# Optimization experiments

Hardware: AMD Instinct MI355X
Metric: run time of the kernel (lower is better)

The kernel has to match this reference:

```python
import jax, jax.numpy as jnp
import numpy as np

B, T, S, D, H, DK, DV = 4, 2048, 2048, 1024, 16, 64, 64


def setup_inputs() -> dict:
    key = jax.random.key(0)
    ks = jax.random.split(key, 12)
    sq = 1.0 / np.sqrt(D)
    return {
        "query": jax.random.normal(ks[0], (B, T, D), jnp.float32),
        "value": jax.random.normal(ks[1], (B, S, D), jnp.float32),
        "mask": jnp.ones((B, T, S), dtype=bool),
        "Wq": jax.random.normal(ks[2], (D, H, DK), jnp.float32) * sq,
        "bq": jnp.zeros((H, DK), jnp.float32),
        "Wk": jax.random.normal(ks[3], (D, H, DK), jnp.float32) * sq,
        "bk": jnp.zeros((H, DK), jnp.float32),
        "Wv": jax.random.normal(ks[4], (D, H, DV), jnp.float32) * sq,
        "bv": jnp.zeros((H, DV), jnp.float32),
        "Wo": jax.random.normal(ks[5], (H, DV, D), jnp.float32) * (1.0 / np.sqrt(H * DV)),
        "bo": jnp.zeros((D,), jnp.float32),
    }


def reference(query, value, mask, Wq, bq, Wk, bk, Wv, bv, Wo, bo):
    # key input defaults to value when only [query, value] is given
    q = jnp.einsum("btd,dhk->bthk", query, Wq) + bq  # [B,T,H,DK]
    k = jnp.einsum("bsd,dhk->bshk", value, Wk) + bk  # [B,S,H,DK]
    v = jnp.einsum("bsd,dhv->bshv", value, Wv) + bv  # [B,S,H,DV]
    # dot_product_equation 'aecd,abcd->acbe': scores[b,h,t,s]
    scores = jnp.einsum("bshk,bthk->bhts", k, q) * (1.0 / np.sqrt(DK))
    # MaskedSoftmax: mask [B,T,S] expanded at axis 1 -> [B,1,T,S]
    adder = (1.0 - mask[:, None, :, :].astype(scores.dtype)) * -10000.0
    probs = jax.nn.softmax(scores + adder, axis=-1)
    # combine_equation 'acbe,aecd->abcd'
    attn = jnp.einsum("bhts,bshv->bthv", probs, v)  # [B,T,H,DV]
    out = jnp.einsum("bthv,hvd->btd", attn, Wo) + bo  # [B,T,D]
    return out
```

## Files before the change

kernel.cpp:

```cpp
#include <hip/hip_runtime.h>

typedef __bf16 bf16x8 __attribute__((ext_vector_type(8)));
typedef __bf16 bf16x4 __attribute__((ext_vector_type(4)));
typedef float  f32x4  __attribute__((ext_vector_type(4)));
typedef int    i32x4  __attribute__((ext_vector_type(4)));

typedef __attribute__((address_space(1))) unsigned int as1_u32;
typedef __attribute__((address_space(3))) unsigned int as3_u32;

#define DEVI __device__ __forceinline__

DEVI unsigned short f2bf(float f) {
    union { float f; unsigned u; } v; v.f = f;
    unsigned r = (v.u + 0x7fffu + ((v.u >> 16) & 1u)) >> 16;
    return (unsigned short)r;
}

DEVI void gload16(const void* g, void* l) {
    __builtin_amdgcn_global_load_lds((const as1_u32*)g, (as3_u32*)l, 16, 0, 0);
}

#define C_EXP 0.18033688011112042f
#define MASK_ADD (-14426.950408889634f)

__global__ __launch_bounds__(256) void cvt_kernel(const float* __restrict__ in,
                                                  unsigned short* __restrict__ out,
                                                  int n8) {
    const int stride = gridDim.x * 256;
    for (int idx = blockIdx.x * 256 + threadIdx.x; idx < n8; idx += stride) {
        const f32x4 a = *(const f32x4*)(in + (size_t)idx * 8);
        const f32x4 b = *(const f32x4*)(in + (size_t)idx * 8 + 4);
        union { bf16x4 v[2]; i32x4 q; } u;
        u.v[0] = __builtin_convertvector(a, bf16x4);
        u.v[1] = __builtin_convertvector(b, bf16x4);
        *(i32x4*)(out + (size_t)idx * 8) = u.q;
    }
}

__global__ __launch_bounds__(256) void wtrans_kernel(const float* __restrict__ W0,
                                                     const float* __restrict__ W1,
                                                     const float* __restrict__ W2,
                                                     const float* __restrict__ W3,
                                                     unsigned short* __restrict__ T0,
                                                     unsigned short* __restrict__ T1,
                                                     unsigned short* __restrict__ T2,
                                                     unsigned short* __restrict__ T3) {
    __shared__ float tile[64][65];
    const float* W;
    unsigned short* WT;
    float scale = 1.0f;
    switch (blockIdx.z) {
        case 0:  W = W0; WT = T0; scale = C_EXP; break;
        case 1:  W = W1; WT = T1; break;
        case 2:  W = W2; WT = T2; break;
        default: W = W3; WT = T3; break;
    }
    const int k0 = blockIdx.x * 64, n0 = blockIdx.y * 64;
    const int i = threadIdx.x;
    const int c4 = (i & 15) * 4, rbase = i >> 4;
    for (int rr = 0; rr < 4; ++rr) {
        const int kl = rbase + rr * 16;
        const float4 v = *(const float4*)(W + (size_t)(k0 + kl) * 1024 + n0 + c4);
        tile[kl][c4 + 0] = v.x; tile[kl][c4 + 1] = v.y;
        tile[kl][c4 + 2] = v.z; tile[kl][c4 + 3] = v.w;
    }
    __syncthreads();
    for (int rr = 0; rr < 4; ++rr) {
        const int nl = rbase + rr * 16;
        ushort4 o;
        o.x = f2bf(tile[c4 + 0][nl] * scale); o.y = f2bf(tile[c4 + 1][nl] * scale);
        o.z = f2bf(tile[c4 + 2][nl] * scale); o.w = f2bf(tile[c4 + 3][nl] * scale);
        *(ushort4*)(WT + (size_t)(n0 + nl) * 1024 + k0 + c4) = o;
    }
}

__global__ __launch_bounds__(256) void maskflag_kernel(const int* __restrict__ mask,
                                                       unsigned* __restrict__ flagsW) {
    const int bid = blockIdx.x;
    const int b = bid >> 9, rem = bid & 511;
    const int tb = rem >> 5, si = rem & 31;
    const int i = threadIdx.x;
    const int t = tb * 128 + (i >> 1);
    const int s = si * 64 + (i & 1) * 32;
    const uint4* p = (const uint4*)(mask + ((size_t)(b * 2048 + t)) * 2048 + s);
    int ok = 1;
    #pragma unroll
    for (int u = 0; u < 8; ++u) {
        const uint4 a = p[u];
        ok &= (a.x != 0) & (a.y != 0) & (a.z != 0) & (a.w != 0);
    }
    int all = __syncthreads_and(ok);
    if (i == 0 && !all) atomicOr(&flagsW[b * 16 + tb], 1u << si);
}

template <int MODE>
__global__ __launch_bounds__(256) void mm_kernel(const unsigned short* __restrict__ A,
                                                 const unsigned short* __restrict__ BT,
                                                 const float* __restrict__ bias,
                                                 float bscale,
                                                 void* __restrict__ Ov) {
    __shared__ __align__(16) unsigned short Ab[128 * 32];
    __shared__ __align__(16) unsigned short Bb[128 * 32];
    const int bid = blockIdx.x;
    const int xcd = bid & 7, jj = bid >> 3;
    const int n0 = (jj & 7) * 128;
    const int m0 = ((jj >> 3) * 8 + xcd) * 128;
    const int i = threadIdx.x, w = i >> 6, l = i & 63;
    const int wm = w >> 1, wn = w & 1;
    const int c = l & 15, g = l >> 4;
    const int rloc = l >> 2;
    const int schunk = ((l & 3) ^ ((l >> 3) & 3)) * 8;
    const int rs = (c >> 1) & 3;

    f32x4 acc[4][4] = {};

    const unsigned short* Asrc = A + (size_t)(m0 + w * 32 + rloc) * 1024 + schunk;
    const unsigned short* Bsrc = BT + (size_t)(n0 + w * 32 + rloc) * 1024 + schunk;
    unsigned short* AbBase = &Ab[(w * 32) * 32];
    unsigned short* BbBase = &Bb[(w * 32) * 32];

    for (int k0 = 0; k0 < 1024; k0 += 32) {
        gload16(Asrc + k0,             AbBase);
        gload16(Asrc + k0 + 16 * 1024, AbBase + 16 * 32);
        gload16(Bsrc + k0,             BbBase);
        gload16(Bsrc + k0 + 16 * 1024, BbBase + 16 * 32);
        __syncthreads();
        bf16x8 af[4], bfr[4];
        #pragma unroll
        for (int mf = 0; mf < 4; ++mf)
            af[mf] = *(const bf16x8*)&Ab[(wm * 64 + mf * 16 + c) * 32 + (g ^ rs) * 8];
        #pragma unroll
        for (int nf = 0; nf < 4; ++nf)
            bfr[nf] = *(const bf16x8*)&Bb[(wn * 64 + nf * 16 + c) * 32 + (g ^ rs) * 8];
        #pragma unroll
        for (int mf = 0; mf < 4; ++mf)
            #pragma unroll
            for (int nf = 0; nf < 4; ++nf)
                acc[mf][nf] = __builtin_amdgcn_mfma_f32_16x16x32_bf16(af[mf], bfr[nf], acc[mf][nf], 0, 0, 0);
        __syncthreads();
    }

    #pragma unroll
    for (int nf = 0; nf < 4; ++nf) {
        const int n = n0 + wn * 64 + nf * 16 + c;
        const float bv = bias[n] * bscale;
        const int h = n >> 6, cc = n & 63;
        #pragma unroll
        for (int mf = 0; mf < 4; ++mf) {
            const int mbase = m0 + wm * 64 + mf * 16 + g * 4;
            if (MODE == 0) {
                const int b = mbase >> 11, t = mbase & 2047;
                unsigned short* O = (unsigned short*)Ov;
                #pragma unroll
                for (int r = 0; r < 4; ++r)
                    O[(((size_t)(b * 16 + h)) * 2048 + t + r) * 64 + cc] = f2bf(acc[mf][nf][r] + bv);
            } else if (MODE == 1) {
                const int b = mbase >> 11, t = mbase & 2047;
                f32x4 v;
                #pragma unroll
                for (int r = 0; r < 4; ++r) v[r] = acc[mf][nf][r] + bv;
                bf16x4 pv = __builtin_convertvector(v, bf16x4);
                unsigned short* O = (unsigned short*)Ov;
                *(bf16x4*)(O + (((size_t)(b * 16 + h)) * 64 + cc) * 2048 + t) = pv;
            } else {
                float* O = (float*)Ov;
                #pragma unroll
                for (int r = 0; r < 4; ++r)
                    O[(size_t)(mbase + r) * 1024 + n] = acc[mf][nf][r] + bv;
            }
        }
    }
}

__global__ __launch_bounds__(256, 5) void attn_kernel(const unsigned short* __restrict__ Qp,
                                                      const unsigned short* __restrict__ Kp,
                                                      const unsigned short* __restrict__ VTp,
                                                      const int* __restrict__ mask,
                                                      const unsigned* __restrict__ flagsW,
                                                      unsigned short* __restrict__ attnb) {
    __shared__ __align__(16) unsigned short Kt[2][64 * 64];
    __shared__ __align__(16) unsigned short Vt[2][64 * 64];

    const int bid = blockIdx.x;
    const int xcd = bid & 7, jj = bid >> 3;
    const int bh = xcd * 8 + (jj >> 5);
    const int tb = jj & 31;
    const int b = bh >> 4, h = bh & 15;
    const int i = threadIdx.x, w = i >> 6, l = i & 63;
    const int c = l & 15, g = l >> 4;

    const unsigned short* Qb  = Qp  + (size_t)bh * 2048 * 64;
    const unsigned short* Kb  = Kp  + (size_t)bh * 2048 * 64;
    const unsigned short* VTb = VTp + (size_t)bh * 64 * 2048;

    const int twave = tb * 64 + w * 16;

    const unsigned notall = __builtin_amdgcn_readfirstlane(flagsW[b * 16 + (tb >> 1)]);

    bf16x8 qf[2];
    #pragma unroll
    for (int kq = 0; kq < 2; ++kq)
        qf[kq] = *(const bf16x8*)(Qb + (size_t)(twave + c) * 64 + kq * 32 + g * 8);

    f32x4 o[4] = {};
    f32x4 dacc = {};

    bf16x8 ones8;
    #pragma unroll
    for (int j = 0; j < 8; ++j) ones8[j] = (__bf16)1.0f;

    int rrow[4], rswz[4];
    #pragma unroll
    for (int sm = 0; sm < 4; ++sm) {
        rrow[sm] = (sm >> 1) * 32 + (c >> 2) * 8 + (sm & 1) * 4 + (c & 3);
        rswz[sm] = (rrow[sm] ^ (rrow[sm] >> 2)) & 7;
    }
    int vswz[4];
    #pragma unroll
    for (int vm = 0; vm < 4; ++vm) {
        const int rv = vm * 16 + c;
        vswz[vm] = (rv ^ (rv >> 2)) & 7;
    }

    const int srow = l >> 3, sslot = l & 7;

    const unsigned short* kstage[2];
    const unsigned short* vstage[2];
    #pragma unroll
    for (int u = 0; u < 2; ++u) {
        const int row = w * 16 + u * 8 + srow;
        const int ch = sslot ^ ((row ^ (row >> 2)) & 7);
        gload16(Kb + (size_t)row * 64 + ch * 8, &Kt[0][(w * 16 + u * 8) * 64]);
        gload16(VTb + (size_t)row * 2048 + ch * 8, &Vt[0][(w * 16 + u * 8) * 64]);
        kstage[u] = Kb + (size_t)(64 + row) * 64 + ch * 8;
        vstage[u] = VTb + (size_t)row * 2048 + 64 + ch * 8;
    }
    __syncthreads();

    #pragma unroll 2
    for (int it = 0; it < 32; ++it) {
        const int buf = it & 1;
        const int s0 = it * 64;

        if (it < 31) {
            #pragma unroll
            for (int u = 0; u < 2; ++u) {
                gload16(kstage[u], &Kt[buf ^ 1][(w * 16 + u * 8) * 64]);
                gload16(vstage[u], &Vt[buf ^ 1][(w * 16 + u * 8) * 64]);
                kstage[u] += 64 * 64;
                vstage[u] += 64;
            }
        }

        f32x4 sc[4] = {};
        __builtin_amdgcn_s_setprio(1);
        #pragma unroll
        for (int sm = 0; sm < 4; ++sm)
            #pragma unroll
            for (int kq = 0; kq < 2; ++kq) {
                const bf16x8 kf = *(const bf16x8*)&Kt[buf][rrow[sm] * 64 + (((kq * 4 + g) ^ rswz[sm]) * 8)];
                sc[sm] = __builtin_amdgcn_mfma_f32_16x16x32_bf16(kf, qf[kq], sc[sm], 0, 0, 0);
            }
        __builtin_amdgcn_s_setprio(0);

        if (notall & (1u << it)) {
            #pragma unroll
            for (int sm = 0; sm < 4; ++sm)
                #pragma unroll
                for (int r = 0; r < 4; ++r) {
                    const int t = twave + c;
                    const int s = s0 + (sm >> 1) * 32 + g * 8 + (sm & 1) * 4 + r;
                    if (mask[(size_t)(b * 2048 + t) * 2048 + s] == 0) sc[sm][r] += MASK_ADD;
                }
        }

        bf16x8 pa[2];
        #pragma unroll
        for (int kv = 0; kv < 2; ++kv) {
            f32x4 p0, p1;
            #pragma unroll
            for (int r = 0; r < 4; ++r) {
                p0[r] = __builtin_amdgcn_exp2f(sc[kv * 2][r]);
                p1[r] = __builtin_amdgcn_exp2f(sc[kv * 2 + 1][r]);
            }
            union { struct { bf16x4 lo, hi; } h; bf16x8 v; } u;
            u.h.lo = __builtin_convertvector(p0, bf16x4);
            u.h.hi = __builtin_convertvector(p1, bf16x4);
            pa[kv] = u.v;
        }

        __builtin_amdgcn_s_setprio(1);
        #pragma unroll
        for (int kv = 0; kv < 2; ++kv) {
            dacc = __builtin_amdgcn_mfma_f32_16x16x32_bf16(ones8, pa[kv], dacc, 0, 0, 0);
            #pragma unroll
            for (int vm = 0; vm < 4; ++vm) {
                const bf16x8 vf = *(const bf16x8*)&Vt[buf][(vm * 16 + c) * 64 + (((kv * 4 + g) ^ vswz[vm]) * 8)];
                o[vm] = __builtin_amdgcn_mfma_f32_16x16x32_bf16(vf, pa[kv], o[vm], 0, 0, 0);
            }
        }
        __builtin_amdgcn_s_setprio(0);

        __syncthreads();
    }

    const float inv = 1.0f / dacc[0];

    const int t = twave + c;
    #pragma unroll
    for (int vm = 0; vm < 4; ++vm) {
        f32x4 v4;
        #pragma unroll
        for (int r = 0; r < 4; ++r) v4[r] = o[vm][r] * inv;
        bf16x4 pv = __builtin_convertvector(v4, bf16x4);
        *(bf16x4*)(attnb + (size_t)(b * 2048 + t) * 1024 + h * 64 + vm * 16 + g * 4) = pv;
    }
}

extern "C" void kernel_launch(void* const* d_in, const int* in_sizes, int n_in,
                              void* d_out, int out_size, void* d_ws, size_t ws_size,
                              hipStream_t stream) {
    const float* query = (const float*)d_in[0];
    const float* value = (const float*)d_in[1];
    const int*   mask  = (const int*)d_in[2];
    const float* Wq = (const float*)d_in[3];
    const float* bq = (const float*)d_in[4];
    const float* Wk = (const float*)d_in[5];
    const float* bk = (const float*)d_in[6];
    const float* Wv = (const float*)d_in[7];
    const float* bv = (const float*)d_in[8];
    const float* Wo = (const float*)d_in[9];
    const float* bo = (const float*)d_in[10];

    char* ws = (char*)d_ws;
    unsigned short* WqT   = (unsigned short*)(ws + ((size_t)0  << 20));
    unsigned short* WkT   = (unsigned short*)(ws + ((size_t)2  << 20));
    unsigned short* WvT   = (unsigned short*)(ws + ((size_t)4  << 20));
    unsigned short* WoT   = (unsigned short*)(ws + ((size_t)6  << 20));
    unsigned*       flagsW= (unsigned*)      (ws + ((size_t)8  << 20));
    unsigned short* CONV  = (unsigned short*)(ws + ((size_t)9  << 20));
    unsigned short* Qp    = (unsigned short*)(ws + ((size_t)25 << 20));
    unsigned short* Kp    = (unsigned short*)(ws + ((size_t)41 << 20));
    unsigned short* VTp   = (unsigned short*)(ws + ((size_t)57 << 20));

    const int n8 = 8192 * 1024 / 8;

    hipMemsetAsync(flagsW, 0, 64 * sizeof(unsigned), stream);

    cvt_kernel<<<2048, 256, 0, stream>>>(value, CONV, n8);
    wtrans_kernel<<<dim3(16, 16, 4), 256, 0, stream>>>(Wq, Wk, Wv, Wo, WqT, WkT, WvT, WoT);
    maskflag_kernel<<<2048, 256, 0, stream>>>(mask, flagsW);
    mm_kernel<0><<<512, 256, 0, stream>>>(CONV, WkT, bk, 1.0f, Kp);
    mm_kernel<1><<<512, 256, 0, stream>>>(CONV, WvT, bv, 1.0f, VTp);

    cvt_kernel<<<2048, 256, 0, stream>>>(query, CONV, n8);
    mm_kernel<0><<<512, 256, 0, stream>>>(CONV, WqT, bq, C_EXP, Qp);

    attn_kernel<<<2048, 256, 0, stream>>>(Qp, Kp, VTp, mask, flagsW, CONV);

    mm_kernel<2><<<512, 256, 0, stream>>>(CONV, WoT, bo, 1.0f, (float*)d_out);
}
```

Before: 224.2 us.

## Process two query row-tiles per wave in attention to reuse K/V fragments

Each wave now handles 32 query rows (two 16-row sub-tiles) instead of 16, so every K and V fragment read from LDS feeds two MFMAs. The attention grid is halved to 1024 blocks and the launch-bounds occupancy hint drops from 5 to 4 to make room for the doubled accumulators. This is meant to cut LDS read traffic and global K/V staging per query row, at the cost of higher register pressure and fewer resident waves to hide latency.

```diff
diff --git a/kernel.cpp b/kernel.cpp
--- a/kernel.cpp
+++ b/kernel.cpp
@@ -172,7 +172,7 @@
     }
 }
 
-__global__ __launch_bounds__(256, 5) void attn_kernel(const unsigned short* __restrict__ Qp,
+__global__ __launch_bounds__(256, 4) void attn_kernel(const unsigned short* __restrict__ Qp,
                                                       const unsigned short* __restrict__ Kp,
                                                       const unsigned short* __restrict__ VTp,
                                                       const int* __restrict__ mask,
@@ -183,8 +183,8 @@
 
     const int bid = blockIdx.x;
     const int xcd = bid & 7, jj = bid >> 3;
-    const int bh = xcd * 8 + (jj >> 5);
-    const int tb = jj & 31;
+    const int bh = xcd * 8 + (jj >> 4);
+    const int tb = jj & 15;
     const int b = bh >> 4, h = bh & 15;
     const int i = threadIdx.x, w = i >> 6, l = i & 63;
     const int c = l & 15, g = l >> 4;
@@ -193,17 +193,21 @@
     const unsigned short* Kb  = Kp  + (size_t)bh * 2048 * 64;
     const unsigned short* VTb = VTp + (size_t)bh * 64 * 2048;
 
-    const int twave = tb * 64 + w * 16;
-
-    const unsigned notall = __builtin_amdgcn_readfirstlane(flagsW[b * 16 + (tb >> 1)]);
-
-    bf16x8 qf[2];
-    #pragma unroll
-    for (int kq = 0; kq < 2; ++kq)
-        qf[kq] = *(const bf16x8*)(Qb + (size_t)(twave + c) * 64 + kq * 32 + g * 8);
-
-    f32x4 o[4] = {};
-    f32x4 dacc = {};
+    const int twave = tb * 128 + w * 32;
+    const int tA = twave + c, tB = twave + 16 + c;
+
+    const unsigned notall = __builtin_amdgcn_readfirstlane(flagsW[b * 16 + tb]);
+
+    bf16x8 qfA[2], qfB[2];
+    #pragma unroll
+    for (int kq = 0; kq < 2; ++kq) {
+        qfA[kq] = *(const bf16x8*)(Qb + (size_t)tA * 64 + kq * 32 + g * 8);
+        qfB[kq] = *(const bf16x8*)(Qb + (size_t)tB * 64 + kq * 32 + g * 8);
+    }
+
+    f32x4 oA[4] = {}, oB[4] = {};
+    f32x4 daccA = {}, daccB = {};
+    const f32x4 zf = {};
 
     bf16x8 ones8;
     #pragma unroll
@@ -252,15 +256,22 @@
             }
         }
 
-        f32x4 sc[4] = {};
+        f32x4 scA[4], scB[4];
         __builtin_amdgcn_s_setprio(1);
         #pragma unroll
-        for (int sm = 0; sm < 4; ++sm)
+        for (int sm = 0; sm < 4; ++sm) {
             #pragma unroll
             for (int kq = 0; kq < 2; ++kq) {
                 const bf16x8 kf = *(const bf16x8*)&Kt[buf][rrow[sm] * 64 + (((kq * 4 + g) ^ rswz[sm]) * 8)];
-                sc[sm] = __builtin_amdgcn_mfma_f32_16x16x32_bf16(kf, qf[kq], sc[sm], 0, 0, 0);
-            }
+                if (kq == 0) {
+                    scA[sm] = __builtin_amdgcn_mfma_f32_16x16x32_bf16(kf, qfA[0], zf, 0, 0, 0);
+                    scB[sm] = __builtin_amdgcn_mfma_f32_16x16x32_bf16(kf, qfB[0], zf, 0, 0, 0);
+                } else {
+                    scA[sm] = __builtin_amdgcn_mfma_f32_16x16x32_bf16(kf, qfA[1], scA[sm], 0, 0, 0);
+                    scB[sm] = __builtin_amdgcn_mfma_f32_16x16x32_bf16(kf, qfB[1], scB[sm], 0, 0, 0);
+                }
+            }
+        }
         __builtin_amdgcn_s_setprio(0);
 
         if (notall & (1u << it)) {
@@ -268,35 +279,42 @@
             for (int sm = 0; sm < 4; ++sm)
                 #pragma unroll
                 for (int r = 0; r < 4; ++r) {
-                    const int t = twave + c;
                     const int s = s0 + (sm >> 1) * 32 + g * 8 + (sm & 1) * 4 + r;
-                    if (mask[(size_t)(b * 2048 + t) * 2048 + s] == 0) sc[sm][r] += MASK_ADD;
+                    if (mask[(size_t)(b * 2048 + tA) * 2048 + s] == 0) scA[sm][r] += MASK_ADD;
+                    if (mask[(size_t)(b * 2048 + tB) * 2048 + s] == 0) scB[sm][r] += MASK_ADD;
                 }
         }
 
-        bf16x8 pa[2];
+        bf16x8 paA[2], paB[2];
         #pragma unroll
         for (int kv = 0; kv < 2; ++kv) {
-            f32x4 p0, p1;
+            f32x4 a0, a1, b0, b1;
             #pragma unroll
             for (int r = 0; r < 4; ++r) {
-                p0[r] = __builtin_amdgcn_exp2f(sc[kv * 2][r]);
-                p1[r] = __builtin_amdgcn_exp2f(sc[kv * 2 + 1][r]);
-            }
-            union { struct { bf16x4 lo, hi; } h; bf16x8 v; } u;
-            u.h.lo = __builtin_convertvector(p0, bf16x4);
-            u.h.hi = __builtin_convertvector(p1, bf16x4);
-            pa[kv] = u.v;
+                a0[r] = __builtin_amdgcn_exp2f(scA[kv * 2][r]);
+                a1[r] = __builtin_amdgcn_exp2f(scA[kv * 2 + 1][r]);
+                b0[r] = __builtin_amdgcn_exp2f(scB[kv * 2][r]);
+                b1[r] = __builtin_amdgcn_exp2f(scB[kv * 2 + 1][r]);
+            }
+            union { struct { bf16x4 lo, hi; } hh; bf16x8 v; } ua, ub;
+            ua.hh.lo = __builtin_convertvector(a0, bf16x4);
+            ua.hh.hi = __builtin_convertvector(a1, bf16x4);
+            ub.hh.lo = __builtin_convertvector(b0, bf16x4);
+            ub.hh.hi = __builtin_convertvector(b1, bf16x4);
+            paA[kv] = ua.v;
+            paB[kv] = ub.v;
         }
 
         __builtin_amdgcn_s_setprio(1);
         #pragma unroll
         for (int kv = 0; kv < 2; ++kv) {
-            dacc = __builtin_amdgcn_mfma_f32_16x16x32_bf16(ones8, pa[kv], dacc, 0, 0, 0);
+            daccA = __builtin_amdgcn_mfma_f32_16x16x32_bf16(ones8, paA[kv], daccA, 0, 0, 0);
+            daccB = __builtin_amdgcn_mfma_f32_16x16x32_bf16(ones8, paB[kv], daccB, 0, 0, 0);
             #pragma unroll
             for (int vm = 0; vm < 4; ++vm) {
                 const bf16x8 vf = *(const bf16x8*)&Vt[buf][(vm * 16 + c) * 64 + (((kv * 4 + g) ^ vswz[vm]) * 8)];
-                o[vm] = __builtin_amdgcn_mfma_f32_16x16x32_bf16(vf, pa[kv], o[vm], 0, 0, 0);
+                oA[vm] = __builtin_amdgcn_mfma_f32_16x16x32_bf16(vf, paA[kv], oA[vm], 0, 0, 0);
+                oB[vm] = __builtin_amdgcn_mfma_f32_16x16x32_bf16(vf, paB[kv], oB[vm], 0, 0, 0);
             }
         }
         __builtin_amdgcn_s_setprio(0);
@@ -304,16 +322,18 @@
         __syncthreads();
     }
 
-    const float inv = 1.0f / dacc[0];
-
-    const int t = twave + c;
+    const float invA = 1.0f / daccA[0];
+    const float invB = 1.0f / daccB[0];
+
     #pragma unroll
     for (int vm = 0; vm < 4; ++vm) {
-        f32x4 v4;
-        #pragma unroll
-        for (int r = 0; r < 4; ++r) v4[r] = o[vm][r] * inv;
-        bf16x4 pv = __builtin_convertvector(v4, bf16x4);
-        *(bf16x4*)(attnb + (size_t)(b * 2048 + t) * 1024 + h * 64 + vm * 16 + g * 4) = pv;
+        f32x4 vA, vB;
+        #pragma unroll
+        for (int r = 0; r < 4; ++r) { vA[r] = oA[vm][r] * invA; vB[r] = oB[vm][r] * invB; }
+        bf16x4 pA = __builtin_convertvector(vA, bf16x4);
+        bf16x4 pB = __builtin_convertvector(vB, bf16x4);
+        *(bf16x4*)(attnb + (size_t)(b * 2048 + tA) * 1024 + h * 64 + vm * 16 + g * 4) = pA;
+        *(bf16x4*)(attnb + (size_t)(b * 2048 + tB) * 1024 + h * 64 + vm * 16 + g * 4) = pB;
     }
 }
 
@@ -356,7 +376,7 @@
     cvt_kernel<<<2048, 256, 0, stream>>>(query, CONV, n8);
     mm_kernel<0><<<512, 256, 0, stream>>>(CONV, WqT, bq, C_EXP, Qp);
 
-    attn_kernel<<<2048, 256, 0, stream>>>(Qp, Kp, VTp, mask, flagsW, CONV);
+    attn_kernel<<<1024, 256, 0, stream>>>(Qp, Kp, VTp, mask, flagsW, CONV);
 
     mm_kernel<2><<<512, 256, 0, stream>>>(CONV, WoT, bo, 1.0f, (float*)d_out);
 }
```

Result: faster. 217.6 us (-3.0%).
